# Performance work log

Measured on AMD Instinct MI355X. Metric: run time of the kernel, lower is better.

## Reference

```python
import jax, jax.numpy as jnp
import numpy as np

TAG_SIZE = 50
START = TAG_SIZE - 2  # index of '<START>'
STOP = TAG_SIZE - 1   # index of '<STOP>'
B, S = 64, 512


def setup_inputs() -> dict:
    key = jax.random.key(0)
    k1, k2, k3 = jax.random.split(key, 3)
    feats = jax.random.normal(k1, (B, S, TAG_SIZE), dtype=jnp.float32)
    mask = jnp.ones((B, S), dtype=jnp.int32)
    tags = jax.random.randint(k2, (B, S), 0, START)  # valid tags exclude START/STOP
    transitions = jax.random.normal(k3, (TAG_SIZE, TAG_SIZE), dtype=jnp.float32)
    return {"feats": feats, "mask": mask, "tags": tags, "transitions": transitions}


def reference(feats, mask, tags, transitions):
    """CRF neg_log_likelihood_loss = forward_score (log partition, summed) - gold_score.
    feats: (B,S,T) emissions; mask: (B,S) {0,1}; tags: (B,S) gold tags;
    transitions[i,j] = score of transitioning from tag i to tag j.
    """
    b, s, t = feats.shape
    maskf = mask.astype(feats.dtype)

    # ---- forward algorithm (log partition) via scan over time ----
    feats_t = jnp.swapaxes(feats, 0, 1)            # (S,B,T)
    mask_t = jnp.swapaxes(mask, 0, 1).astype(bool)  # (S,B)
    # t=0: partition[b,j] = feats[b,0,j] + transitions[START, j]
    partition0 = feats_t[0] + transitions[START][None, :]  # (B,T)

    def step(partition, xs):
        f_t, m_t = xs  # (B,T), (B,)
        # cur_values[b,i,j] = partition[b,i] + transitions[i,j] + feats[b,t,j]
        cur_values = partition[:, :, None] + transitions[None, :, :] + f_t[:, None, :]
        cur = jax.nn.logsumexp(cur_values, axis=1)  # (B,T) logsumexp over prev tag
        new_partition = jnp.where(m_t[:, None], cur, partition)
        return new_partition, None

    partition, _ = jax.lax.scan(step, partition0, (feats_t[1:], mask_t[1:]))
    terminal = jax.nn.logsumexp(partition[:, :, None] + transitions[None, :, :], axis=1)  # (B,T)
    forward_score = terminal[:, STOP].sum()

    # ---- gold score ----
    # prev tag at step 0 is START, otherwise tags[:, t-1]
    prev = jnp.concatenate([jnp.full((b, 1), START, dtype=tags.dtype), tags[:, :-1]], axis=1)
    emit = jnp.take_along_axis(feats, tags[..., None], axis=2)[..., 0]  # (B,S)
    trans = transitions[prev, tags]                                      # (B,S)
    tg_energy = ((emit + trans) * maskf).sum()
    lengths = mask.astype(jnp.int32).sum(axis=1)                         # (B,)
    end_ids = jnp.take_along_axis(tags, (lengths - 1)[:, None].astype(tags.dtype), axis=1)[:, 0]
    end_energy = transitions[end_ids, STOP].sum()
    gold_score = tg_energy + end_energy

    return forward_score - gold_score
```

## Files before the change

### kernel.cpp

```cpp
#include <hip/hip_runtime.h>
#include <hip/hip_bf16.h>

#define T 50
#define NB 64
#define NS 512
#define START_TAG 48
#define STOP_TAG 49

typedef _Float16 f16_t;
typedef _Float16 f16x2 __attribute__((ext_vector_type(2)));
typedef _Float16 f16x4 __attribute__((ext_vector_type(4)));
typedef _Float16 f16x8 __attribute__((ext_vector_type(8)));
typedef float    f32x4 __attribute__((ext_vector_type(4)));

static constexpr float LOG2E = 1.4426950408889634f;
static constexpr float LN2F  = 0.6931471805599453f;
static constexpr float S_E   = 6.0f;
#define NEG_BIG (-1.0e38f)

__device__ __forceinline__ float fexp2(float x) { return __builtin_amdgcn_exp2f(x); }
__device__ __forceinline__ float flog2(float x) { return __builtin_amdgcn_logf(x); }
__device__ __forceinline__ f16x2 bcast_h2(f16x2 v, int src) {
    unsigned u = __builtin_amdgcn_readlane(__builtin_bit_cast(unsigned, v), src);
    return __builtin_bit_cast(f16x2, u);
}
__device__ __forceinline__ f16x2 pack_h2(float a, float b) {
    return __builtin_bit_cast(f16x2, __builtin_amdgcn_cvt_pkrtz(a, b));
}

__device__ __forceinline__ float wave_fmax_dpp(float x) {
#define DPP_STEP(ctrl)                                                        \
    do {                                                                      \
        int _s = __builtin_bit_cast(int, x);                                  \
        int _p = __builtin_amdgcn_update_dpp(_s, _s, (ctrl), 0xf, 0xf, false);\
        x = fmaxf(x, __builtin_bit_cast(float, _p));                          \
    } while (0)
    DPP_STEP(0x111);
    DPP_STEP(0x112);
    DPP_STEP(0x114);
    DPP_STEP(0x118);
    DPP_STEP(0x142);
    DPP_STEP(0x143);
#undef DPP_STEP
    return __builtin_bit_cast(float,
        __builtin_amdgcn_readlane(__builtin_bit_cast(int, x), 63));
}

template<int NCHT, int CHLT>
__global__ __launch_bounds__(256, 8)
void crf_chunk(const float* __restrict__ feats, const int* __restrict__ mask,
               const float* __restrict__ trans, f16_t* __restrict__ wsCt,
               float* __restrict__ wsD, float* __restrict__ out, int out_size) {
    const int c    = blockIdx.x;
    const int b    = blockIdx.y;
    const int tid  = threadIdx.x;
    const int w    = tid >> 6;
    const int lane = tid & 63;
    const int l15  = lane & 15;
    const int q    = lane >> 4;

    constexpr int EF_BYTES = 2 * 2 * 64 * 16;
    constexpr int SF_BYTES = CHLT * 64 * 4;
    constexpr int ML_BYTES = 64 * 72 * 2;
    constexpr int SM_BYTES = (EF_BYTES + SF_BYTES) > ML_BYTES
                           ? (EF_BYTES + SF_BYTES) : ML_BYTES;
    __shared__ unsigned char smem[SM_BYTES];
    f16_t* Ef = (f16_t*)smem;
    float (*sF)[64] = (float (*)[64])(smem + EF_BYTES);

    const int t0  = c * CHLT + 1;
    const int nst = (NS - t0 < CHLT) ? (NS - t0) : CHLT;

    f16x4 Afr[2][4];
    #pragma unroll
    for (int kb = 0; kb < 2; kb++)
        #pragma unroll
        for (int mb = 0; mb < 4; mb++) {
            f16x4 v;
            #pragma unroll
            for (int j = 0; j < 4; j++) {
                const int kk = 16 * kb + 4 * q + j;
                const int mm = 16 * mb + l15;
                float x = 0.f;
                if (kk < T && mm < T) x = fexp2(fmaf(trans[kk * T + mm], LOG2E, -S_E));
                v[j] = (f16_t)x;
            }
            Afr[kb][mb] = v;
        }

    {
        const int sidx = tid;
        const int kbr = sidx >> 7;
        const int mbp = (sidx >> 6) & 1;
        const int ln  = sidx & 63;
        const int qq  = ln >> 4;
        const int ll  = ln & 15;
        f16_t* slot = Ef + sidx * 8;
        #pragma unroll
        for (int e = 0; e < 2; e++)
            #pragma unroll
            for (int j = 0; j < 4; j++) {
                const int kk = 16 * (kbr + 2) + 4 * qq + j;
                const int mm = 16 * (2 * mbp + e) + ll;
                float x = 0.f;
                if (kk < T && mm < T) x = fexp2(fmaf(trans[kk * T + mm], LOG2E, -S_E));
                slot[e * 4 + j] = (f16_t)x;
            }
    }

    for (int r = w; r < CHLT; r += 4) {
        int tl = t0 + r; tl = tl < NS ? tl : NS - 1;
        float fv = (lane < T && r < nst) ? feats[((size_t)b * NS + tl) * T + lane] : 0.f;
        sF[r][lane] = (lane < T && r < nst) ? fexp2(fv * LOG2E) : 0.f;
    }

    unsigned long long bm;
    {
        int tl = t0 + lane; tl = tl < NS ? tl : NS - 1;
        int mv = (lane < nst) ? mask[b * NS + tl] : 0;
        bm = __ballot(mv != 0);
    }
    __syncthreads();

    f16x4 Bt[4];
    #pragma unroll
    for (int rb = 0; rb < 4; rb++) {
        f16x4 v;
        #pragma unroll
        for (int j = 0; j < 4; j++)
            v[j] = (f16_t)((rb == w && 4 * q + j == l15) ? 1.f : 0.f);
        Bt[rb] = v;
    }

    float D  = 0.f;
    float m1 = 1.f, m2 = 1.f;
    const f16x8* EfL = (const f16x8*)Ef;

    for (int s = 0; s < nst; s++) {
        if ((bm >> s) & 1ull) {
            int ebits = (int)((__float_as_uint(m2) >> 23) & 255) - 127;
            ebits = ebits > 14 ? 14 : (ebits < -14 ? -14 : ebits);
            const float descale = __uint_as_float((unsigned)(127 - ebits) << 23);
            D += (float)ebits + S_E;

            const f32x4 zz = {0.f, 0.f, 0.f, 0.f};
            f32x4 acc[4];
            #pragma unroll
            for (int mb = 0; mb < 4; mb++)
                acc[mb] = __builtin_amdgcn_mfma_f32_16x16x16f16(Afr[0][mb], Bt[0], zz, 0, 0, 0);
            #pragma unroll
            for (int mb = 0; mb < 4; mb++)
                acc[mb] = __builtin_amdgcn_mfma_f32_16x16x16f16(Afr[1][mb], Bt[1], acc[mb], 0, 0, 0);
            #pragma unroll
            for (int kbr = 0; kbr < 2; kbr++) {
                f16x8 p0 = EfL[(kbr * 2 + 0) * 64 + lane];
                f16x8 p1 = EfL[(kbr * 2 + 1) * 64 + lane];
                acc[0] = __builtin_amdgcn_mfma_f32_16x16x16f16(__builtin_shufflevector(p0, p0, 0,1,2,3), Bt[2 + kbr], acc[0], 0, 0, 0);
                acc[1] = __builtin_amdgcn_mfma_f32_16x16x16f16(__builtin_shufflevector(p0, p0, 4,5,6,7), Bt[2 + kbr], acc[1], 0, 0, 0);
                acc[2] = __builtin_amdgcn_mfma_f32_16x16x16f16(__builtin_shufflevector(p1, p1, 0,1,2,3), Bt[2 + kbr], acc[2], 0, 0, 0);
                acc[3] = __builtin_amdgcn_mfma_f32_16x16x16f16(__builtin_shufflevector(p1, p1, 4,5,6,7), Bt[2 + kbr], acc[3], 0, 0, 0);
            }

            f16x2 wmax2 = {(f16_t)0.f, (f16_t)0.f};
            #pragma unroll
            for (int mb = 0; mb < 4; mb++) {
                f32x4 cs = *(const f32x4*)&sF[s][16 * mb + 4 * q];
                float v0 = acc[mb][0] * (cs[0] * descale);
                float v1 = acc[mb][1] * (cs[1] * descale);
                float v2 = acc[mb][2] * (cs[2] * descale);
                float v3 = acc[mb][3] * (cs[3] * descale);
                f16x4 hv;
                hv[0] = (f16_t)v0; hv[1] = (f16_t)v1;
                hv[2] = (f16_t)v2; hv[3] = (f16_t)v3;
                Bt[mb] = hv;
                f16x2 lo = __builtin_shufflevector(hv, hv, 0, 1);
                f16x2 hi = __builtin_shufflevector(hv, hv, 2, 3);
                wmax2 = __builtin_elementwise_max(wmax2,
                          __builtin_elementwise_max(lo, hi));
            }
            float wm = fmaxf((float)wmax2[0], (float)wmax2[1]);

            m2 = m1;
            m1 = wave_fmax_dpp(wm);
        }
    }

    __syncthreads();
    {
        f16_t* Ml = (f16_t*)smem;
        const int P2 = 72;
        #pragma unroll
        for (int rb = 0; rb < 4; rb++) {
            f16x4 v = Bt[rb];
            #pragma unroll
            for (int r = 0; r < 4; r++)
                Ml[(16 * rb + 4 * q + r) * P2 + 16 * w + l15] = v[r];
        }
        __syncthreads();
        const int row = tid >> 2;
        const int seg = tid & 3;
        const f16_t* src = &Ml[row * P2 + seg * 16];
        f16_t* dst = wsCt + ((size_t)(b * NCHT + c)) * 4096 + row * 64 + seg * 16;
        ((int4*)dst)[0] = *(const int4*)&src[0];
        ((int4*)dst)[1] = *(const int4*)&src[8];
    }
    if (lane == 0) wsD[(b * NCHT + c) * 4 + w] = D;

    if (c == 0 && b == 0 && tid < out_size) out[tid] = 0.f;
}

template<int NCHT>
__global__ __launch_bounds__(128, 1)
void crf_combine(const float* __restrict__ feats, const int* __restrict__ mask,
                 const int* __restrict__ tags, const float* __restrict__ trans,
                 const f16_t* __restrict__ wsCt, const float* __restrict__ wsD,
                 float* __restrict__ out) {
    const int b    = blockIdx.x;
    const int tid  = threadIdx.x;
    const int wv   = tid >> 6;
    const int lane = tid & 63;

    __shared__ float sGold;
    float fwd = 0.f;

    if (wv == 1) {
        float gsum = 0.f;
        int   lcnt = 0;
        for (int s = lane; s < NS; s += 64) {
            int   m  = mask[b * NS + s];
            int   tg = tags[b * NS + s];
            int   pv = (s == 0) ? START_TAG : tags[b * NS + s - 1];
            float e  = feats[((size_t)b * NS + s) * T + tg];
            float tr = trans[pv * T + tg];
            if (m) { gsum += e + tr; lcnt += 1; }
        }
        #pragma unroll
        for (int off = 32; off > 0; off >>= 1) {
            gsum += __shfl_down(gsum, off, 64);
            lcnt += __shfl_down(lcnt, off, 64);
        }
        if (lane == 0) sGold = gsum + trans[tags[b * NS + lcnt - 1] * T + STOP_TAG];
    } else {
        float part = (lane < T)
            ? (feats[(size_t)b * NS * T + lane] + trans[START_TAG * T + lane]) * LOG2E
            : NEG_BIG;

        float Dq[NCHT];
        #pragma unroll
        for (int cc = 0; cc < NCHT; cc++)
            Dq[cc] = wsD[(b * NCHT + cc) * 4 + (lane >> 4)];

        int bX[32], bY[32], bZ[32];

        auto ld = [&](int (&buf)[32], int cc) {
            const f16_t* src = wsCt + (size_t)(b * NCHT + cc) * 4096 + lane * 64;
            #pragma unroll
            for (int kk = 0; kk < 8; kk++)
                *(int4*)&buf[4 * kk] = ((const int4*)src)[kk];
        };

        auto body = [&](int (&cur)[32], int cc) {
            float tmp = part + Dq[cc];
            float sft = wave_fmax_dpp(tmp);
            float ex  = fexp2(tmp - sft);
            float exo = __shfl_xor(ex, 1, 64);
            f16x2 pk  = pack_h2(ex, exo);

            float a0 = 0.f, a1 = 0.f, a2 = 0.f, a3 = 0.f;
            #pragma unroll
            for (int k = 0; k < 25; k += 4) {
                a0 = __builtin_amdgcn_fdot2(bcast_h2(pk, 2 * k), __builtin_bit_cast(f16x2, cur[k]), a0, false);
                if (k + 1 < 25) a1 = __builtin_amdgcn_fdot2(bcast_h2(pk, 2 * (k + 1)), __builtin_bit_cast(f16x2, cur[k + 1]), a1, false);
                if (k + 2 < 25) a2 = __builtin_amdgcn_fdot2(bcast_h2(pk, 2 * (k + 2)), __builtin_bit_cast(f16x2, cur[k + 2]), a2, false);
                if (k + 3 < 25) a3 = __builtin_amdgcn_fdot2(bcast_h2(pk, 2 * (k + 3)), __builtin_bit_cast(f16x2, cur[k + 3]), a3, false);
            }
            part = sft + flog2((a0 + a1) + (a2 + a3));
        };

        ld(bX, 0);
        if (1 < NCHT) ld(bY, 1);
        #pragma unroll
        for (int g = 0; g < NCHT; g += 3) {
            { if (g + 2 < NCHT) ld(bZ, g + 2); body(bX, g); }
            if (g + 1 < NCHT) { if (g + 3 < NCHT) ld(bX, g + 3); body(bY, g + 1); }
            if (g + 2 < NCHT) { if (g + 4 < NCHT) ld(bY, g + 4); body(bZ, g + 2); }
        }

        float v = (lane < T) ? part + trans[lane * T + STOP_TAG] * LOG2E : NEG_BIG;
        float mx = wave_fmax_dpp(v);
        float ee = (lane < T) ? fexp2(v - mx) : 0.f;
        #pragma unroll
        for (int off = 32; off > 0; off >>= 1) ee += __shfl_xor(ee, off, 64);
        fwd = (mx + flog2(ee)) * LN2F;
    }

    __syncthreads();
    if (tid == 0) atomicAdd(out, fwd - sGold);
}

extern "C" void kernel_launch(void* const* d_in, const int* in_sizes, int n_in,
                              void* d_out, int out_size, void* d_ws, size_t ws_size,
                              hipStream_t stream) {
    const float* feats = (const float*)d_in[0];
    const int*   mask  = (const int*)d_in[1];
    const int*   tags  = (const int*)d_in[2];
    const float* trans = (const float*)d_in[3];
    float* out = (float*)d_out;


    const size_t matBytes32 = (size_t)NB * 32 * 4096 * sizeof(f16_t);
    const size_t need32     = matBytes32 + (size_t)NB * 32 * 4 * sizeof(float);
    const size_t matBytes16 = (size_t)NB * 16 * 4096 * sizeof(f16_t);
    const size_t need16     = matBytes16 + (size_t)NB * 16 * 4 * sizeof(float);

    if (ws_size >= need32) {
        f16_t* wsCt = (f16_t*)d_ws;
        float* wsD  = (float*)((char*)d_ws + matBytes32);
        crf_chunk<32, 16><<<dim3(32, NB), 256, 0, stream>>>(feats, mask, trans, wsCt, wsD, out, out_size);
        crf_combine<32><<<NB, 128, 0, stream>>>(feats, mask, tags, trans, wsCt, wsD, out);
    } else if (ws_size >= need16) {
        f16_t* wsCt = (f16_t*)d_ws;
        float* wsD  = (float*)((char*)d_ws + matBytes16);
        crf_chunk<16, 32><<<dim3(16, NB), 256, 0, stream>>>(feats, mask, trans, wsCt, wsD, out, out_size);
        crf_combine<16><<<NB, 128, 0, stream>>>(feats, mask, tags, trans, wsCt, wsD, out);
    } else {
        const size_t matBytes8 = (size_t)NB * 8 * 4096 * sizeof(f16_t);
        f16_t* wsCt = (f16_t*)d_ws;
        float* wsD  = (float*)((char*)d_ws + matBytes8);
        crf_chunk<8, 64><<<dim3(8, NB), 256, 0, stream>>>(feats, mask, trans, wsCt, wsD, out, out_size);
        crf_combine<8><<<NB, 128, 0, stream>>>(feats, mask, tags, trans, wsCt, wsD, out);
    }
}
```

Before: 110.7 us.

## Stream chunk matrices through LDS with async global_load_lds pipeline

Result: no change. 112.5 us (+1.6%).

```diff
diff --git a/kernel.cpp b/kernel.cpp
--- a/kernel.cpp
+++ b/kernel.cpp
@@ -26,6 +26,12 @@
 }
 __device__ __forceinline__ f16x2 pack_h2(float a, float b) {
     return __builtin_bit_cast(f16x2, __builtin_amdgcn_cvt_pkrtz(a, b));
+}
+
+__device__ __forceinline__ void gload_lds16(const void* g, void* l) {
+    __builtin_amdgcn_global_load_lds(
+        (const __attribute__((address_space(1))) void*)g,
+        (__attribute__((address_space(3))) void*)l, 16, 0, 0);
 }
 
 __device__ __forceinline__ float wave_fmax_dpp(float x) {
@@ -219,7 +225,9 @@
     const int tid  = threadIdx.x;
     const int wv   = tid >> 6;
     const int lane = tid & 63;
-
+    constexpr int G = NCHT / 2;
+
+    __shared__ f16_t sBuf[4 * 14 * 512];
     __shared__ float sGold;
     float fwd = 0.f;
 
@@ -250,16 +258,20 @@
         for (int cc = 0; cc < NCHT; cc++)
             Dq[cc] = wsD[(b * NCHT + cc) * 4 + (lane >> 4)];
 
-        int bX[32], bY[32], bZ[32];
-
-        auto ld = [&](int (&buf)[32], int cc) {
-            const f16_t* src = wsCt + (size_t)(b * NCHT + cc) * 4096 + lane * 64;
-            #pragma unroll
-            for (int kk = 0; kk < 8; kk++)
-                *(int4*)&buf[4 * kk] = ((const int4*)src)[kk];
+        auto issueGroup = [&](int g) {
+            const int slot = g & 3;
+            #pragma unroll
+            for (int i = 0; i < 2; i++) {
+                const int cc = 2 * g + i;
+                const f16_t* srcRow = wsCt + (size_t)(b * NCHT + cc) * 4096 + lane * 64;
+                #pragma unroll
+                for (int t = 0; t < 7; t++)
+                    gload_lds16(srcRow + t * 8,
+                                &sBuf[(size_t)(slot * 14 + i * 7 + t) * 512]);
+            }
         };
 
-        auto body = [&](int (&cur)[32], int cc) {
+        auto body = [&](int cc, int cur[28]) {
             float tmp = part + Dq[cc];
             float sft = wave_fmax_dpp(tmp);
             float ex  = fexp2(tmp - sft);
@@ -277,13 +289,30 @@
             part = sft + flog2((a0 + a1) + (a2 + a3));
         };
 
-        ld(bX, 0);
-        if (1 < NCHT) ld(bY, 1);
-        #pragma unroll
-        for (int g = 0; g < NCHT; g += 3) {
-            { if (g + 2 < NCHT) ld(bZ, g + 2); body(bX, g); }
-            if (g + 1 < NCHT) { if (g + 3 < NCHT) ld(bX, g + 3); body(bY, g + 1); }
-            if (g + 2 < NCHT) { if (g + 4 < NCHT) ld(bY, g + 4); body(bZ, g + 2); }
+        issueGroup(0);
+        if (1 < G) issueGroup(1);
+        if (2 < G) issueGroup(2);
+
+        #pragma unroll
+        for (int g = 0; g < G; g++) {
+            if (g + 3 < G) issueGroup(g + 3);
+            const int ahead = (G - 1 - g) < 3 ? (G - 1 - g) : 3;
+            if (ahead == 3)      asm volatile("s_waitcnt vmcnt(42)" ::: "memory");
+            else if (ahead == 2) asm volatile("s_waitcnt vmcnt(28)" ::: "memory");
+            else if (ahead == 1) asm volatile("s_waitcnt vmcnt(14)" ::: "memory");
+            else                 asm volatile("s_waitcnt vmcnt(0)"  ::: "memory");
+            __builtin_amdgcn_sched_barrier(0);
+
+            #pragma unroll
+            for (int i = 0; i < 2; i++) {
+                const int cc = 2 * g + i;
+                int cur[28];
+                const int base = ((g & 3) * 14 + i * 7) * 512 + lane * 8;
+                #pragma unroll
+                for (int t = 0; t < 7; t++)
+                    *(int4*)&cur[4 * t] = *(const int4*)&sBuf[base + t * 512];
+                body(cc, cur);
+            }
         }
 
         float v = (lane < T) ? part + trans[lane * T + STOP_TAG] * LOG2E : NEG_BIG;
```
